# Optimization experiments

Hardware: AMD Instinct MI355X
Metric: run time of the kernel (lower is better)

## Reference

```python
import jax, jax.numpy as jnp
import numpy as np

EMB = 1024
HID = 4 * EMB
HEADS = 16
HEAD_DIM = EMB // HEADS


def gelu_tanh(x):
    c = jnp.sqrt(jnp.asarray(2.0 / jnp.pi, x.dtype))
    return 0.5 * x * (1.0 + jnp.tanh(c * (x + 0.044715 * x ** 3)))


def layernorm(x, scale, shift, eps=1e-5):
    mean = jnp.mean(x, axis=-1, keepdims=True)
    var = jnp.var(x, axis=-1, keepdims=True)
    return scale * (x - mean) / jnp.sqrt(var + eps) + shift


def setup_inputs() -> dict:
    key = jax.random.key(0)
    ks = jax.random.split(key, 12)
    s = 0.02
    return {
        "x": jax.random.normal(ks[0], (2, 2048, EMB), jnp.float32),
        "Wq": jax.random.normal(ks[1], (EMB, EMB), jnp.float32) * s,
        "Wk": jax.random.normal(ks[2], (EMB, EMB), jnp.float32) * s,
        "Wv": jax.random.normal(ks[3], (EMB, EMB), jnp.float32) * s,
        "Wo": jax.random.normal(ks[4], (EMB, EMB), jnp.float32) * s,
        "bo": jnp.zeros((EMB,), jnp.float32),
        "W1": jax.random.normal(ks[5], (EMB, HID), jnp.float32) * s,
        "b1": jnp.zeros((HID,), jnp.float32),
        "W2": jax.random.normal(ks[6], (HID, EMB), jnp.float32) * s,
        "b2": jnp.zeros((EMB,), jnp.float32),
        "ln1_scale": jnp.ones((EMB,), jnp.float32),
        "ln1_shift": jnp.zeros((EMB,), jnp.float32),
        "ln2_scale": jnp.ones((EMB,), jnp.float32),
        "ln2_shift": jnp.zeros((EMB,), jnp.float32),
    }


def reference(x, Wq, Wk, Wv, Wo, bo, W1, b1, W2, b2,
              ln1_scale, ln1_shift, ln2_scale, ln2_shift):
    B, S, D = x.shape

    # pre-norm attention + residual
    h = layernorm(x, ln1_scale, ln1_shift)
    q = (h @ Wq).reshape(B, S, HEADS, HEAD_DIM).transpose(0, 2, 1, 3)  # bhsd
    k = (h @ Wk).reshape(B, S, HEADS, HEAD_DIM).transpose(0, 2, 1, 3)
    v = (h @ Wv).reshape(B, S, HEADS, HEAD_DIM).transpose(0, 2, 1, 3)

    scores = jnp.einsum("bhqd,bhkd->bhqk", q, k)
    causal = jnp.tril(jnp.ones((S, S), bool))
    scores = jnp.where(causal, scores, -jnp.inf)
    attn = jax.nn.softmax(scores / jnp.sqrt(jnp.asarray(HEAD_DIM, x.dtype)), axis=-1)
    ctx = jnp.einsum("bhqk,bhkd->bhqd", attn, v)
    ctx = ctx.transpose(0, 2, 1, 3).reshape(B, S, D)
    x = x + (ctx @ Wo + bo)

    # pre-norm FFN + residual
    h = layernorm(x, ln2_scale, ln2_shift)
    h = gelu_tanh(h @ W1 + b1) @ W2 + b2
    return x + h
```

## Files before the change

kernel.cpp:

```cpp
#include <hip/hip_runtime.h>
#include <hip/hip_bf16.h>
#include <stdint.h>

#define B_   2
#define S_   2048
#define D_   1024
#define H_   16
#define DH_  64
#define HID_ 4096
#define M_   4096

typedef __bf16 bf16x8 __attribute__((ext_vector_type(8)));
typedef float  f32x4  __attribute__((ext_vector_type(4)));
typedef float  f32x16 __attribute__((ext_vector_type(16)));
typedef uint32_t u32x4v __attribute__((ext_vector_type(4)));

typedef const uint32_t __attribute__((address_space(1))) u32g;
typedef uint32_t       __attribute__((address_space(3))) u32l;

#define SCL2K_ 0.18033688011112042f

__device__ __forceinline__ uint16_t f2bf(float f) {
  uint32_t u = __builtin_bit_cast(uint32_t, f);
  u += 0x7FFFu + ((u >> 16) & 1u);
  return (uint16_t)(u >> 16);
}

__device__ __forceinline__ float bf2f(uint16_t u) {
  return __builtin_bit_cast(float, (uint32_t)u << 16);
}

__device__ __forceinline__ void gload_lds16(const void* g, void* l) {
  __builtin_amdgcn_global_load_lds((u32g*)g, (u32l*)l, 16, 0, 0);
}

__device__ __forceinline__ const bf16x8* lds8p(const uint16_t* base, int row,
                                               int cole) {
  int byt = (cole * 2) ^ ((row & 7) << 4);
  return reinterpret_cast<const bf16x8*>(base + row * 64 + (byt >> 1));
}

__device__ __forceinline__ const bf16x8* lds8p32(const uint16_t* base, int row,
                                                 int cole) {
  int byt = (cole * 2) ^ ((row & 7) << 4) ^ ((row & 8) << 2);
  return reinterpret_cast<const bf16x8*>(base + row * 64 + (byt >> 1));
}

__device__ __forceinline__ uint32_t cvtpk_bf16(float lo, float hi) {
  uint32_t d;
  asm("v_cvt_pk_bf16_f32 %0, %1, %2" : "=v"(d) : "v"(lo), "v"(hi));
  return d;
}
__device__ __forceinline__ void pl32swap(uint32_t& a, uint32_t& b) {
  asm volatile("v_permlane32_swap_b32 %0, %1" : "+v"(a), "+v"(b));
}

__global__ void wconv_t(const float* __restrict__ W, uint16_t* __restrict__ WT,
                        int K, int N) {
  __shared__ float tile[32][33];
  int n0 = blockIdx.x * 32, k0 = blockIdx.y * 32;
  int tx = threadIdx.x, ty = threadIdx.y;
#pragma unroll
  for (int i = 0; i < 4; ++i)
    tile[ty + i * 8][tx] = W[(size_t)(k0 + ty + i * 8) * N + n0 + tx];
  __syncthreads();
#pragma unroll
  for (int i = 0; i < 4; ++i)
    WT[(size_t)(n0 + ty + i * 8) * K + k0 + tx] = f2bf(tile[tx][ty + i * 8]);
}

__global__ __launch_bounds__(256) void ln_k(const float* __restrict__ x,
                                            const float* __restrict__ sc,
                                            const float* __restrict__ sh,
                                            uint16_t* __restrict__ out) {
  int row = blockIdx.x;
  int t = threadIdx.x;
  float4 v = reinterpret_cast<const float4*>(x + (size_t)row * D_)[t];
  float s = v.x + v.y + v.z + v.w;
  float ss = v.x * v.x + v.y * v.y + v.z * v.z + v.w * v.w;
#pragma unroll
  for (int off = 32; off >= 1; off >>= 1) {
    s += __shfl_xor(s, off);
    ss += __shfl_xor(ss, off);
  }
  __shared__ float red[8];
  int wid = t >> 6, lane = t & 63;
  if (lane == 0) { red[wid] = s; red[wid + 4] = ss; }
  __syncthreads();
  s = red[0] + red[1] + red[2] + red[3];
  ss = red[4] + red[5] + red[6] + red[7];
  float mean = s * (1.0f / D_);
  float var = ss * (1.0f / D_) - mean * mean;
  float rstd = rsqrtf(var + 1e-5f);
  float4 g = reinterpret_cast<const float4*>(sc)[t];
  float4 b = reinterpret_cast<const float4*>(sh)[t];
  ushort4 o;
  o.x = f2bf(g.x * (v.x - mean) * rstd + b.x);
  o.y = f2bf(g.y * (v.y - mean) * rstd + b.y);
  o.z = f2bf(g.z * (v.z - mean) * rstd + b.z);
  o.w = f2bf(g.w * (v.w - mean) * rstd + b.w);
  reinterpret_cast<ushort4*>(out + (size_t)row * D_)[t] = o;
}

__global__ __launch_bounds__(256) void reduce4_k(
    const uint16_t* __restrict__ P0, const uint16_t* __restrict__ P1,
    const uint16_t* __restrict__ P2, const uint16_t* __restrict__ P3,
    const float* __restrict__ resid, const float* __restrict__ bias,
    float* __restrict__ out) {
  int row = blockIdx.x, t = threadIdx.x;
  size_t base = (size_t)row * D_ + t * 4;
  float4 r = *reinterpret_cast<const float4*>(resid + base);
  float4 b = reinterpret_cast<const float4*>(bias)[t];
  ushort4 u0 = *reinterpret_cast<const ushort4*>(P0 + base);
  ushort4 u1 = *reinterpret_cast<const ushort4*>(P1 + base);
  ushort4 u2 = *reinterpret_cast<const ushort4*>(P2 + base);
  ushort4 u3 = *reinterpret_cast<const ushort4*>(P3 + base);
  float4 o;
  o.x = r.x + b.x + bf2f(u0.x) + bf2f(u1.x) + bf2f(u2.x) + bf2f(u3.x);
  o.y = r.y + b.y + bf2f(u0.y) + bf2f(u1.y) + bf2f(u2.y) + bf2f(u3.y);
  o.z = r.z + b.z + bf2f(u0.z) + bf2f(u1.z) + bf2f(u2.z) + bf2f(u3.z);
  o.w = r.w + b.w + bf2f(u0.w) + bf2f(u1.w) + bf2f(u2.w) + bf2f(u3.w);
  *reinterpret_cast<float4*>(out + base) = o;
}

__global__ void vtrans_k(const uint16_t* __restrict__ V, uint16_t* __restrict__ VT) {
  __shared__ uint16_t tile[32][33];
  int s0 = blockIdx.x * 32, d0 = blockIdx.y * 32, bh = blockIdx.z;
  int tx = threadIdx.x, ty = threadIdx.y;
  const uint16_t* vb = V + (size_t)bh * S_ * DH_;
  uint16_t* vtb = VT + (size_t)bh * DH_ * S_;
#pragma unroll
  for (int i = 0; i < 4; ++i)
    tile[ty + i * 8][tx] = vb[(size_t)(s0 + ty + i * 8) * DH_ + d0 + tx];
  __syncthreads();
#pragma unroll
  for (int i = 0; i < 4; ++i)
    vtb[(size_t)(d0 + ty + i * 8) * S_ + s0 + tx] = tile[tx][ty + i * 8];
}

template <int EPI>
__global__ __launch_bounds__(512, 2) void gemm8(
    const uint16_t* __restrict__ A, const uint16_t* __restrict__ BT,
    void* __restrict__ Cout, const float* __restrict__ bias,
    uint16_t* __restrict__ P0, uint16_t* __restrict__ P1,
    uint16_t* __restrict__ P2, uint16_t* __restrict__ P3,
    int M, int N, int K) {
  __shared__ uint16_t As[2][2][128 * 64];
  __shared__ uint16_t Bs[2][2][128 * 64];
  int t = threadIdx.x;
  int lane = t & 63, wid = t >> 6;
  int wm = wid >> 2, wn = wid & 3;
  int l15 = lane & 15, lk8 = (lane >> 4) * 8, lr4 = (lane >> 4) * 4;
  int gx = gridDim.x;
  int nwg = gx * gridDim.y;
  int bid = blockIdx.y * gx + blockIdx.x;
  int swz = (bid & 7) * (nwg >> 3) + (bid >> 3);
  int bx = swz % gx, by = swz / gx;
  int m0 = by * 256, n0 = bx * 256;
  int ksz = K / gridDim.z;
  int kbeg = blockIdx.z * ksz;
  int NT = ksz >> 6;

  int r0 = t >> 3, slot0 = t & 7;
  int scol = (slot0 ^ (r0 & 7)) * 8;

  auto STAGE_A = [&](int kt, int half, int buf) {
    const uint16_t* src =
        A + (size_t)(m0 + half * 128 + r0) * K + kbeg + kt * 64 + scol;
    uint16_t* dst = &As[buf][half][t * 8];
    gload_lds16(src, dst);
    gload_lds16(src + (size_t)64 * K, dst + 4096);
  };
  auto STAGE_B = [&](int kt, int half, int buf) {
    const uint16_t* src =
        BT + (size_t)(n0 + half * 128 + r0) * K + kbeg + kt * 64 + scol;
    uint16_t* dst = &Bs[buf][half][t * 8];
    gload_lds16(src, dst);
    gload_lds16(src + (size_t)64 * K, dst + 4096);
  };

  bf16x8 a[4][2], b[2][2];
  auto LDA = [&](int buf, int mh) {
#pragma unroll
    for (int j = 0; j < 4; ++j)
#pragma unroll
      for (int kk = 0; kk < 2; ++kk)
        a[j][kk] = *lds8p(As[buf][mh], wm * 64 + j * 16 + l15, kk * 32 + lk8);
  };
  auto LDB = [&](int buf, int nh) {
#pragma unroll
    for (int jj = 0; jj < 2; ++jj)
#pragma unroll
      for (int kk = 0; kk < 2; ++kk)
        b[jj][kk] = *lds8p(Bs[buf][nh], wn * 32 + jj * 16 + l15, kk * 32 + lk8);
  };

  f32x4 acc[8][4] = {};
  auto MM = [&](int mh, int nh) {
    __builtin_amdgcn_s_setprio(1);
#pragma unroll
    for (int kk = 0; kk < 2; ++kk)
#pragma unroll
      for (int j = 0; j < 4; ++j)
#pragma unroll
        for (int jj = 0; jj < 2; ++jj)
          acc[mh * 4 + j][nh * 2 + jj] = __builtin_amdgcn_mfma_f32_16x16x32_bf16(
              a[j][kk], b[jj][kk], acc[mh * 4 + j][nh * 2 + jj], 0, 0, 0);
    __builtin_amdgcn_s_setprio(0);
  };
  auto BAR = [&]() {
    __builtin_amdgcn_s_barrier();
    asm volatile("" ::: "memory");
  };
  auto LGKM0 = [&]() {
    asm volatile("s_waitcnt lgkmcnt(0)" ::: "memory");
    __builtin_amdgcn_sched_barrier(0);
  };

  STAGE_A(0, 0, 0);
  STAGE_B(0, 1, 0);
  STAGE_B(0, 0, 0);
  STAGE_A(0, 1, 0);
  STAGE_A(1, 0, 1);
  STAGE_B(1, 1, 1);
  asm volatile("s_waitcnt vmcnt(4)" ::: "memory");
  BAR();

  for (int T = 0; T < NT; ++T) {
    int cur = T & 1;
    LDA(cur, 0);
    LDB(cur, 0);
    if (T + 1 < NT) STAGE_B(T + 1, 0, cur ^ 1);
    BAR(); LGKM0();
    MM(0, 0);
    BAR();
    LDB(cur, 1);
    if (T + 1 < NT) STAGE_A(T + 1, 1, cur ^ 1);
    BAR(); LGKM0();
    MM(0, 1);
    BAR();
    LDA(cur, 1);
    if (T + 2 < NT) STAGE_A(T + 2, 0, cur);
    BAR(); LGKM0();
    MM(1, 1);
    BAR();
    LDB(cur, 0);
    if (T + 2 < NT) STAGE_B(T + 2, 1, cur);
    BAR(); LGKM0();
    MM(1, 0);
    if (T + 1 < NT) {
      if (T == NT - 2) {
        asm volatile("s_waitcnt vmcnt(0)" ::: "memory");
      } else {
        asm volatile("s_waitcnt vmcnt(4)" ::: "memory");
      }
    }
    BAR();
  }

  uint16_t* Pz = nullptr;
  if constexpr (EPI == 3) {
    int z = blockIdx.z;
    Pz = (z == 0) ? P0 : (z == 1) ? P1 : (z == 2) ? P2 : P3;
  }
#pragma unroll
  for (int mi = 0; mi < 8; ++mi) {
#pragma unroll
    for (int ni = 0; ni < 4; ++ni) {
#pragma unroll
      for (int rr = 0; rr < 4; ++rr) {
        int gm = m0 + (mi >> 2) * 128 + wm * 64 + (mi & 3) * 16 + lr4 + rr;
        int gn = n0 + (ni >> 1) * 128 + wn * 32 + (ni & 1) * 16 + l15;
        float v = acc[mi][ni][rr];
        if constexpr (EPI == 0) {
          int which = gn >> 10, nc = gn & 1023;
          int h = nc >> 6, dh = nc & 63;
          int bb = gm >> 11, s = gm & 2047;
          if (which == 1) v *= SCL2K_;
          ((uint16_t*)Cout)[((size_t)which * 32 + bb * 16 + h) * (S_ * 64) +
                            (size_t)s * 64 + dh] = f2bf(v);
        } else if constexpr (EPI == 2) {
          float u = v + bias[gn];
          float y = 0.7978845608028654f * (u + 0.044715f * u * u * u);
          float e = __expf(2.0f * y);
          float th = 1.0f - 2.0f / (e + 1.0f);
          ((uint16_t*)Cout)[(size_t)gm * N + gn] = f2bf(0.5f * u * (1.0f + th));
        } else {
          Pz[(size_t)gm * N + gn] = f2bf(v);
        }
      }
    }
  }
}

template <int EPI>
__global__ __launch_bounds__(256) void gemm_bt(
    const uint16_t* __restrict__ A, const uint16_t* __restrict__ BT,
    void* __restrict__ Cout, const float* __restrict__ bias,
    const float* __restrict__ resid, int M, int N, int K) {
  __shared__ uint16_t Asm_[128 * 64];
  __shared__ uint16_t Bsm_[128 * 64];
  int t = threadIdx.x;
  int lane = t & 63, wid = t >> 6;
  int wr = wid >> 1, wc = wid & 1;
  int nwg = gridDim.x * gridDim.y;
  int bid = blockIdx.y * gridDim.x + blockIdx.x;
  int swz = (bid & 7) * (nwg >> 3) + (bid >> 3);
  int bx = swz % gridDim.x, by = swz / gridDim.x;
  int m0 = by * 128, n0 = bx * 128;
  int l15 = lane & 15, lk8 = (lane >> 4) * 8;
  f32x4 acc[4][4] = {};

  auto STAGE = [&](int k0) {
#pragma unroll
    for (int it = 0; it < 4; ++it) {
      int idx = it * 256 + t;
      int r = idx >> 3, slot = idx & 7;
      int c = (slot ^ (r & 7)) * 8;
      gload_lds16(A + (size_t)(m0 + r) * K + k0 + c, &Asm_[idx * 8]);
      gload_lds16(BT + (size_t)(n0 + r) * K + k0 + c, &Bsm_[idx * 8]);
    }
  };

  int niter = K >> 6;
  for (int ki = 0; ki < niter; ++ki) {
    __syncthreads();
    STAGE(ki * 64);
    __syncthreads();
#pragma unroll
    for (int kk = 0; kk < 2; ++kk) {
      bf16x8 a[4], b[4];
#pragma unroll
      for (int mi = 0; mi < 4; ++mi)
        a[mi] = *lds8p(Asm_, wr * 64 + mi * 16 + l15, kk * 32 + lk8);
#pragma unroll
      for (int ni = 0; ni < 4; ++ni)
        b[ni] = *lds8p(Bsm_, wc * 64 + ni * 16 + l15, kk * 32 + lk8);
#pragma unroll
      for (int mi = 0; mi < 4; ++mi)
#pragma unroll
        for (int ni = 0; ni < 4; ++ni)
          acc[mi][ni] = __builtin_amdgcn_mfma_f32_16x16x32_bf16(
              a[mi], b[ni], acc[mi][ni], 0, 0, 0);
    }
  }
  int lr4 = (lane >> 4) * 4;
#pragma unroll
  for (int mi = 0; mi < 4; ++mi) {
#pragma unroll
    for (int ni = 0; ni < 4; ++ni) {
#pragma unroll
      for (int r = 0; r < 4; ++r) {
        int gm = m0 + wr * 64 + mi * 16 + lr4 + r;
        int gn = n0 + wc * 64 + ni * 16 + l15;
        float v = acc[mi][ni][r];
        if constexpr (EPI == 1) {
          ((float*)Cout)[(size_t)gm * N + gn] =
              resid[(size_t)gm * N + gn] + v + bias[gn];
        }
      }
    }
  }
}

__global__ __launch_bounds__(64) void attn32_k(const uint16_t* __restrict__ Q,
                                               const uint16_t* __restrict__ Kv,
                                               const uint16_t* __restrict__ VT,
                                               uint16_t* __restrict__ ctx) {
  __shared__ uint16_t Ksm[2][32 * 64];
  __shared__ uint16_t Vsm[2][32 * 64];
  __shared__ float invLDS[32];
  int bid = blockIdx.x;
  int qt = bid >> 5;
  int bh = bid & 31;
  int lane = threadIdx.x;
  int l31 = lane & 31, lh = lane >> 5;
  int b_ = bh >> 4, h_ = bh & 15;

  auto STAGE = [&](int k0, int bufi) {
#pragma unroll
    for (int c = 0; c < 4; ++c) {
      int idx = c * 64 + lane;
      int r = idx >> 3, sl = idx & 7;
      int slp = sl ^ (r & 7) ^ ((r & 8) >> 2);
      gload_lds16(Kv + ((size_t)bh * S_ + k0 + r) * 64 + slp * 8,
                  &Ksm[bufi][idx * 8]);
      int dh = 2 * r + (slp >> 2), ko = (slp & 3) * 8;
      gload_lds16(VT + ((size_t)bh * 64 + dh) * S_ + k0 + ko,
                  &Vsm[bufi][idx * 8]);
    }
  };

  int nkt = qt + 1;
  int qbase = qt * 32;
  bf16x8 qf[4];
#pragma unroll
  for (int dk = 0; dk < 4; ++dk)
    qf[dk] = *reinterpret_cast<const bf16x8*>(
        Q + ((size_t)bh * S_ + qbase + l31) * 64 + dk * 16 + lh * 8);
  f32x16 o0 = {}, o1 = {};
  float mrow = -3.0e38f, lsum = 0.0f;
  int buf = 0;
  STAGE(0, 0);

  for (int t = 0; t < nkt; ++t) {
    if (t + 1 < nkt) {
      STAGE((t + 1) * 32, buf ^ 1);
      asm volatile("s_waitcnt vmcnt(8)" ::: "memory");
    } else {
      asm volatile("s_waitcnt vmcnt(0)" ::: "memory");
    }
    __builtin_amdgcn_sched_barrier(0);
    f32x16 Sf = {};
#pragma unroll
    for (int dk = 0; dk < 4; ++dk) {
      bf16x8 kf = *lds8p32(Ksm[buf], l31, dk * 16 + lh * 8);
      Sf = __builtin_amdgcn_mfma_f32_32x32x16_bf16(kf, qf[dk], Sf, 0, 0, 0);
    }
    float sv[16];
    if (t == nkt - 1) {
#pragma unroll
      for (int rr = 0; rr < 16; ++rr) {
        int koff = (rr & 3) + 8 * (rr >> 2) + 4 * lh;
        sv[rr] = (koff <= l31) ? Sf[rr] : -3.0e38f;
      }
    } else {
#pragma unroll
      for (int rr = 0; rr < 16; ++rr) sv[rr] = Sf[rr];
    }
    float mt16 = sv[0];
#pragma unroll
    for (int rr = 1; rr < 16; ++rr) mt16 = fmaxf(mt16, sv[rr]);
    if (__any(mt16 > mrow + 8.0f)) {
      float mt = mt16;
#pragma unroll
      for (int off = 32; off >= 1; off >>= 1)
        mt = fmaxf(mt, __shfl_xor(mt, off));
      mt = fmaxf(mt, mrow);
      float fac = __builtin_amdgcn_exp2f(mrow - mt);
      mrow = mt;
      lsum *= fac;
#pragma unroll
      for (int rr = 0; rr < 16; ++rr) { o0[rr] *= fac; o1[rr] *= fac; }
    }
    float pv[16];
#pragma unroll
    for (int rr = 0; rr < 16; ++rr) {
      pv[rr] = __builtin_amdgcn_exp2f(sv[rr] - mrow);
      lsum += pv[rr];
    }
    uint32_t a0 = cvtpk_bf16(pv[0], pv[1]), b0 = cvtpk_bf16(pv[4], pv[5]);
    pl32swap(a0, b0);
    uint32_t a1 = cvtpk_bf16(pv[2], pv[3]), b1 = cvtpk_bf16(pv[6], pv[7]);
    pl32swap(a1, b1);
    u32x4v w0 = {a0, a1, b0, b1};
    bf16x8 pa0 = __builtin_bit_cast(bf16x8, w0);
    uint32_t a2 = cvtpk_bf16(pv[8], pv[9]), b2 = cvtpk_bf16(pv[12], pv[13]);
    pl32swap(a2, b2);
    uint32_t a3 = cvtpk_bf16(pv[10], pv[11]), b3 = cvtpk_bf16(pv[14], pv[15]);
    pl32swap(a3, b3);
    u32x4v w1 = {a2, a3, b2, b3};
    bf16x8 pa1 = __builtin_bit_cast(bf16x8, w1);
    int vrow = l31 >> 1, vcb = (l31 & 1) * 32 + lh * 8;
    bf16x8 v00 = *lds8p32(Vsm[buf], vrow, vcb);
    o0 = __builtin_amdgcn_mfma_f32_32x32x16_bf16(pa0, v00, o0, 0, 0, 0);
    bf16x8 v01 = *lds8p32(Vsm[buf], vrow, vcb + 16);
    o0 = __builtin_amdgcn_mfma_f32_32x32x16_bf16(pa1, v01, o0, 0, 0, 0);
    bf16x8 v10 = *lds8p32(Vsm[buf], 16 + vrow, vcb);
    o1 = __builtin_amdgcn_mfma_f32_32x32x16_bf16(pa0, v10, o1, 0, 0, 0);
    bf16x8 v11 = *lds8p32(Vsm[buf], 16 + vrow, vcb + 16);
    o1 = __builtin_amdgcn_mfma_f32_32x32x16_bf16(pa1, v11, o1, 0, 0, 0);
    buf ^= 1;
  }
  lsum += __shfl_xor(lsum, 32);
  if (lane < 32) invLDS[l31] = 1.0f / lsum;
  asm volatile("s_waitcnt lgkmcnt(0)" ::: "memory");
  __builtin_amdgcn_sched_barrier(0);
  float inv[16];
#pragma unroll
  for (int rr = 0; rr < 16; ++rr)
    inv[rr] = invLDS[(rr & 3) + 8 * (rr >> 2) + 4 * lh];
#pragma unroll
  for (int rr = 0; rr < 16; ++rr) {
    int s = qbase + (rr & 3) + 8 * (rr >> 2) + 4 * lh;
    size_t base = ((size_t)(b_ * S_ + s)) * D_ + h_ * 64;
    ctx[base + l31] = f2bf(o0[rr] * inv[rr]);
    ctx[base + 32 + l31] = f2bf(o1[rr] * inv[rr]);
  }
}

extern "C" void kernel_launch(void* const* d_in, const int* in_sizes, int n_in,
                              void* d_out, int out_size, void* d_ws, size_t ws_size,
                              hipStream_t stream) {
  const float* x    = (const float*)d_in[0];
  const float* Wq   = (const float*)d_in[1];
  const float* Wk   = (const float*)d_in[2];
  const float* Wv   = (const float*)d_in[3];
  const float* Wo   = (const float*)d_in[4];
  const float* bo   = (const float*)d_in[5];
  const float* W1   = (const float*)d_in[6];
  const float* b1   = (const float*)d_in[7];
  const float* W2   = (const float*)d_in[8];
  const float* b2   = (const float*)d_in[9];
  const float* ln1s = (const float*)d_in[10];
  const float* ln1b = (const float*)d_in[11];
  const float* ln2s = (const float*)d_in[12];
  const float* ln2b = (const float*)d_in[13];
  float* out = (float*)d_out;
  char* ws = (char*)d_ws;

  const size_t MB = 1024 * 1024;
  uint16_t* WQKVT = (uint16_t*)(ws + 0);
  uint16_t* WOT   = (uint16_t*)(ws + 6 * MB);
  uint16_t* W1T   = (uint16_t*)(ws + 8 * MB);
  uint16_t* W2T   = (uint16_t*)(ws + 16 * MB);
  uint16_t* H1    = (uint16_t*)(ws + 24 * MB);
  float*    X1    = (float*)(ws + 32 * MB);
  uint16_t* QKV   = (uint16_t*)(ws + 48 * MB);
  uint16_t* VTb   = (uint16_t*)(ws + 72 * MB);
  uint16_t* CTX   = (uint16_t*)(ws + 80 * MB);
  uint16_t* FFH   = (uint16_t*)(ws + 48 * MB);
  uint16_t* SP0   = (uint16_t*)(ws + 0);
  uint16_t* SP1   = (uint16_t*)(ws + 8 * MB);
  uint16_t* SP2   = (uint16_t*)(ws + 24 * MB);
  uint16_t* SP3   = (uint16_t*)(ws + 80 * MB);

  dim3 b32x8(32, 8);
  wconv_t<<<dim3(32, 32), b32x8, 0, stream>>>(Wq, WQKVT, 1024, 1024);
  wconv_t<<<dim3(32, 32), b32x8, 0, stream>>>(Wk, WQKVT + 1024 * 1024, 1024, 1024);
  wconv_t<<<dim3(32, 32), b32x8, 0, stream>>>(Wv, WQKVT + 2 * 1024 * 1024, 1024, 1024);
  wconv_t<<<dim3(32, 32), b32x8, 0, stream>>>(Wo, WOT, 1024, 1024);
  wconv_t<<<dim3(128, 32), b32x8, 0, stream>>>(W1, W1T, 1024, 4096);
  wconv_t<<<dim3(32, 128), b32x8, 0, stream>>>(W2, W2T, 4096, 1024);

  ln_k<<<M_, 256, 0, stream>>>(x, ln1s, ln1b, H1);
  gemm8<0><<<dim3(12, 16), 512, 0, stream>>>(H1, WQKVT, QKV, nullptr,
                                             nullptr, nullptr, nullptr, nullptr,
                                             M_, 3072, 1024);
  const uint16_t* Qp = QKV;
  const uint16_t* Kp = QKV + (size_t)32 * S_ * 64;
  const uint16_t* Vp = QKV + (size_t)64 * S_ * 64;
  vtrans_k<<<dim3(64, 2, 32), b32x8, 0, stream>>>(Vp, VTb);
  attn32_k<<<dim3(2048), 64, 0, stream>>>(Qp, Kp, VTb, CTX);
  gemm_bt<1><<<dim3(8, 32), 256, 0, stream>>>(CTX, WOT, X1, bo, x, M_, 1024, 1024);
  ln_k<<<M_, 256, 0, stream>>>(X1, ln2s, ln2b, H1);
  gemm8<2><<<dim3(16, 16), 512, 0, stream>>>(H1, W1T, FFH, b1,
                                             nullptr, nullptr, nullptr, nullptr,
                                             M_, 4096, 1024);
  gemm8<3><<<dim3(4, 16, 4), 512, 0, stream>>>(FFH, W2T, nullptr, nullptr,
                                               SP0, SP1, SP2, SP3,
                                               M_, 1024, 4096);
  reduce4_k<<<M_, 256, 0, stream>>>(SP0, SP1, SP2, SP3, X1, b2, out);
}
```

Baseline: 256.5 us.

## Split causal attention KV range across two blocks and merge partials; fuse weight conversions

Attention now splits each query tile's causal key range into two halves handled by separate blocks. Each block writes an unnormalized bf16 partial output plus its row max and sum, and a new combine kernel merges the pairs, which balances the triangular workload and doubles the block count. The attention loop also drops LDS staging in favour of direct register loads of K and V, double-buffered in registers. The six weight-transpose launches are merged into one kernel. The cost is an extra launch and round-trip of the partial outputs, plus rounding the unnormalized partials to bf16.

```diff
diff --git a/kernel.cpp b/kernel.cpp
--- a/kernel.cpp
+++ b/kernel.cpp
@@ -40,12 +40,6 @@
   return reinterpret_cast<const bf16x8*>(base + row * 64 + (byt >> 1));
 }
 
-__device__ __forceinline__ const bf16x8* lds8p32(const uint16_t* base, int row,
-                                                 int cole) {
-  int byt = (cole * 2) ^ ((row & 7) << 4) ^ ((row & 8) << 2);
-  return reinterpret_cast<const bf16x8*>(base + row * 64 + (byt >> 1));
-}
-
 __device__ __forceinline__ uint32_t cvtpk_bf16(float lo, float hi) {
   uint32_t d;
   asm("v_cvt_pk_bf16_f32 %0, %1, %2" : "=v"(d) : "v"(lo), "v"(hi));
@@ -55,10 +49,29 @@
   asm volatile("v_permlane32_swap_b32 %0, %1" : "+v"(a), "+v"(b));
 }
 
-__global__ void wconv_t(const float* __restrict__ W, uint16_t* __restrict__ WT,
-                        int K, int N) {
+__global__ void wconv_all(const float* __restrict__ Wq, const float* __restrict__ Wk,
+                          const float* __restrict__ Wv, const float* __restrict__ Wo,
+                          const float* __restrict__ W1, const float* __restrict__ W2,
+                          uint16_t* __restrict__ WQKVT, uint16_t* __restrict__ WOT,
+                          uint16_t* __restrict__ W1T, uint16_t* __restrict__ W2T) {
   __shared__ float tile[32][33];
-  int n0 = blockIdx.x * 32, k0 = blockIdx.y * 32;
+  int idx = blockIdx.x;
+  const float* W;
+  uint16_t* WT;
+  int K, N, within;
+  if (idx < 4096) {
+    int which = idx >> 10;
+    within = idx & 1023;
+    W = (which == 0) ? Wq : (which == 1) ? Wk : (which == 2) ? Wv : Wo;
+    WT = (which == 3) ? WOT : WQKVT + (size_t)which * 1024 * 1024;
+    K = 1024; N = 1024;
+  } else if (idx < 8192) {
+    within = idx - 4096; W = W1; WT = W1T; K = 1024; N = 4096;
+  } else {
+    within = idx - 8192; W = W2; WT = W2T; K = 4096; N = 1024;
+  }
+  int nb = N >> 5;
+  int n0 = (within % nb) * 32, k0 = (within / nb) * 32;
   int tx = threadIdx.x, ty = threadIdx.y;
 #pragma unroll
   for (int i = 0; i < 4; ++i)
@@ -363,129 +376,158 @@
   }
 }
 
-__global__ __launch_bounds__(64) void attn32_k(const uint16_t* __restrict__ Q,
-                                               const uint16_t* __restrict__ Kv,
-                                               const uint16_t* __restrict__ VT,
-                                               uint16_t* __restrict__ ctx) {
-  __shared__ uint16_t Ksm[2][32 * 64];
-  __shared__ uint16_t Vsm[2][32 * 64];
-  __shared__ float invLDS[32];
+__global__ __launch_bounds__(64) void attn32s_k(const uint16_t* __restrict__ Q,
+                                                const uint16_t* __restrict__ Kv,
+                                                const uint16_t* __restrict__ VT,
+                                                uint16_t* __restrict__ Obuf,
+                                                float* __restrict__ ML) {
   int bid = blockIdx.x;
-  int qt = bid >> 5;
   int bh = bid & 31;
+  int s = (bid >> 5) & 1;
+  int qt = bid >> 6;
   int lane = threadIdx.x;
   int l31 = lane & 31, lh = lane >> 5;
-  int b_ = bh >> 4, h_ = bh & 15;
-
-  auto STAGE = [&](int k0, int bufi) {
-#pragma unroll
-    for (int c = 0; c < 4; ++c) {
-      int idx = c * 64 + lane;
-      int r = idx >> 3, sl = idx & 7;
-      int slp = sl ^ (r & 7) ^ ((r & 8) >> 2);
-      gload_lds16(Kv + ((size_t)bh * S_ + k0 + r) * 64 + slp * 8,
-                  &Ksm[bufi][idx * 8]);
-      int dh = 2 * r + (slp >> 2), ko = (slp & 3) * 8;
-      gload_lds16(VT + ((size_t)bh * 64 + dh) * S_ + k0 + ko,
-                  &Vsm[bufi][idx * 8]);
-    }
-  };
-
   int nkt = qt + 1;
-  int qbase = qt * 32;
-  bf16x8 qf[4];
-#pragma unroll
-  for (int dk = 0; dk < 4; ++dk)
-    qf[dk] = *reinterpret_cast<const bf16x8*>(
-        Q + ((size_t)bh * S_ + qbase + l31) * 64 + dk * 16 + lh * 8);
+  int h = (nkt + 1) >> 1;
+  int t0 = s ? h : 0, t1 = s ? nkt : h;
+  int pb = ((qt * 32 + bh) << 1) + s;
+
   f32x16 o0 = {}, o1 = {};
   float mrow = -3.0e38f, lsum = 0.0f;
-  int buf = 0;
-  STAGE(0, 0);
-
-  for (int t = 0; t < nkt; ++t) {
-    if (t + 1 < nkt) {
-      STAGE((t + 1) * 32, buf ^ 1);
-      asm volatile("s_waitcnt vmcnt(8)" ::: "memory");
-    } else {
-      asm volatile("s_waitcnt vmcnt(0)" ::: "memory");
+
+  const uint16_t* Kb = Kv + (size_t)bh * S_ * 64;
+  const uint16_t* Vb = VT + (size_t)bh * 64 * S_;
+
+  auto LOADKV = [&](int t, bf16x8 (&kf)[4], bf16x8 (&vf)[4]) {
+    const uint16_t* kp = Kb + (size_t)(t * 32 + l31) * 64 + lh * 8;
+#pragma unroll
+    for (int dk = 0; dk < 4; ++dk)
+      kf[dk] = *reinterpret_cast<const bf16x8*>(kp + dk * 16);
+    const uint16_t* vp = Vb + (size_t)l31 * S_ + t * 32 + lh * 8;
+    vf[0] = *reinterpret_cast<const bf16x8*>(vp);
+    vf[1] = *reinterpret_cast<const bf16x8*>(vp + 16);
+    vf[2] = *reinterpret_cast<const bf16x8*>(vp + 32 * S_);
+    vf[3] = *reinterpret_cast<const bf16x8*>(vp + 32 * S_ + 16);
+  };
+
+  if (t0 < t1) {
+    int qbase = qt * 32;
+    bf16x8 qf[4];
+#pragma unroll
+    for (int dk = 0; dk < 4; ++dk)
+      qf[dk] = *reinterpret_cast<const bf16x8*>(
+          Q + ((size_t)bh * S_ + qbase + l31) * 64 + dk * 16 + lh * 8);
+
+    auto COMPUTE = [&](int t, bf16x8 (&kf)[4], bf16x8 (&vf)[4]) {
+      f32x16 Sf = {};
+#pragma unroll
+      for (int dk = 0; dk < 4; ++dk)
+        Sf = __builtin_amdgcn_mfma_f32_32x32x16_bf16(kf[dk], qf[dk], Sf, 0, 0, 0);
+      float sv[16];
+      if (t == qt) {
+#pragma unroll
+        for (int rr = 0; rr < 16; ++rr) {
+          int koff = (rr & 3) + 8 * (rr >> 2) + 4 * lh;
+          sv[rr] = (koff <= l31) ? Sf[rr] : -3.0e38f;
+        }
+      } else {
+#pragma unroll
+        for (int rr = 0; rr < 16; ++rr) sv[rr] = Sf[rr];
+      }
+      float mt16 = sv[0];
+#pragma unroll
+      for (int rr = 1; rr < 16; ++rr) mt16 = fmaxf(mt16, sv[rr]);
+      if (__any(mt16 > mrow + 8.0f)) {
+        float mt = mt16;
+#pragma unroll
+        for (int off = 32; off >= 1; off >>= 1)
+          mt = fmaxf(mt, __shfl_xor(mt, off));
+        mt = fmaxf(mt, mrow);
+        float fac = __builtin_amdgcn_exp2f(mrow - mt);
+        mrow = mt;
+        lsum *= fac;
+#pragma unroll
+        for (int rr = 0; rr < 16; ++rr) { o0[rr] *= fac; o1[rr] *= fac; }
+      }
+      float pv[16];
+#pragma unroll
+      for (int rr = 0; rr < 16; ++rr) {
+        pv[rr] = __builtin_amdgcn_exp2f(sv[rr] - mrow);
+        lsum += pv[rr];
+      }
+      uint32_t a0 = cvtpk_bf16(pv[0], pv[1]), b0 = cvtpk_bf16(pv[4], pv[5]);
+      pl32swap(a0, b0);
+      uint32_t a1 = cvtpk_bf16(pv[2], pv[3]), b1 = cvtpk_bf16(pv[6], pv[7]);
+      pl32swap(a1, b1);
+      u32x4v w0 = {a0, a1, b0, b1};
+      bf16x8 pa0 = __builtin_bit_cast(bf16x8, w0);
+      uint32_t a2 = cvtpk_bf16(pv[8], pv[9]), b2 = cvtpk_bf16(pv[12], pv[13]);
+      pl32swap(a2, b2);
+      uint32_t a3 = cvtpk_bf16(pv[10], pv[11]), b3 = cvtpk_bf16(pv[14], pv[15]);
+      pl32swap(a3, b3);
+      u32x4v w1 = {a2, a3, b2, b3};
+      bf16x8 pa1 = __builtin_bit_cast(bf16x8, w1);
+      o0 = __builtin_amdgcn_mfma_f32_32x32x16_bf16(pa0, vf[0], o0, 0, 0, 0);
+      o0 = __builtin_amdgcn_mfma_f32_32x32x16_bf16(pa1, vf[1], o0, 0, 0, 0);
+      o1 = __builtin_amdgcn_mfma_f32_32x32x16_bf16(pa0, vf[2], o1, 0, 0, 0);
+      o1 = __builtin_amdgcn_mfma_f32_32x32x16_bf16(pa1, vf[3], o1, 0, 0, 0);
+    };
+
+    bf16x8 kA[4], vA[4], kB[4], vB[4];
+    LOADKV(t0, kA, vA);
+    int t = t0;
+    while (t < t1) {
+      if (t + 1 < t1) LOADKV(t + 1, kB, vB);
+      COMPUTE(t, kA, vA);
+      ++t;
+      if (t >= t1) break;
+      if (t + 1 < t1) LOADKV(t + 1, kA, vA);
+      COMPUTE(t, kB, vB);
+      ++t;
     }
-    __builtin_amdgcn_sched_barrier(0);
-    f32x16 Sf = {};
-#pragma unroll
-    for (int dk = 0; dk < 4; ++dk) {
-      bf16x8 kf = *lds8p32(Ksm[buf], l31, dk * 16 + lh * 8);
-      Sf = __builtin_amdgcn_mfma_f32_32x32x16_bf16(kf, qf[dk], Sf, 0, 0, 0);
-    }
-    float sv[16];
-    if (t == nkt - 1) {
-#pragma unroll
-      for (int rr = 0; rr < 16; ++rr) {
-        int koff = (rr & 3) + 8 * (rr >> 2) + 4 * lh;
-        sv[rr] = (koff <= l31) ? Sf[rr] : -3.0e38f;
-      }
-    } else {
-#pragma unroll
-      for (int rr = 0; rr < 16; ++rr) sv[rr] = Sf[rr];
-    }
-    float mt16 = sv[0];
-#pragma unroll
-    for (int rr = 1; rr < 16; ++rr) mt16 = fmaxf(mt16, sv[rr]);
-    if (__any(mt16 > mrow + 8.0f)) {
-      float mt = mt16;
-#pragma unroll
-      for (int off = 32; off >= 1; off >>= 1)
-        mt = fmaxf(mt, __shfl_xor(mt, off));
-      mt = fmaxf(mt, mrow);
-      float fac = __builtin_amdgcn_exp2f(mrow - mt);
-      mrow = mt;
-      lsum *= fac;
-#pragma unroll
-      for (int rr = 0; rr < 16; ++rr) { o0[rr] *= fac; o1[rr] *= fac; }
-    }
-    float pv[16];
-#pragma unroll
-    for (int rr = 0; rr < 16; ++rr) {
-      pv[rr] = __builtin_amdgcn_exp2f(sv[rr] - mrow);
-      lsum += pv[rr];
-    }
-    uint32_t a0 = cvtpk_bf16(pv[0], pv[1]), b0 = cvtpk_bf16(pv[4], pv[5]);
-    pl32swap(a0, b0);
-    uint32_t a1 = cvtpk_bf16(pv[2], pv[3]), b1 = cvtpk_bf16(pv[6], pv[7]);
-    pl32swap(a1, b1);
-    u32x4v w0 = {a0, a1, b0, b1};
-    bf16x8 pa0 = __builtin_bit_cast(bf16x8, w0);
-    uint32_t a2 = cvtpk_bf16(pv[8], pv[9]), b2 = cvtpk_bf16(pv[12], pv[13]);
-    pl32swap(a2, b2);
-    uint32_t a3 = cvtpk_bf16(pv[10], pv[11]), b3 = cvtpk_bf16(pv[14], pv[15]);
-    pl32swap(a3, b3);
-    u32x4v w1 = {a2, a3, b2, b3};
-    bf16x8 pa1 = __builtin_bit_cast(bf16x8, w1);
-    int vrow = l31 >> 1, vcb = (l31 & 1) * 32 + lh * 8;
-    bf16x8 v00 = *lds8p32(Vsm[buf], vrow, vcb);
-    o0 = __builtin_amdgcn_mfma_f32_32x32x16_bf16(pa0, v00, o0, 0, 0, 0);
-    bf16x8 v01 = *lds8p32(Vsm[buf], vrow, vcb + 16);
-    o0 = __builtin_amdgcn_mfma_f32_32x32x16_bf16(pa1, v01, o0, 0, 0, 0);
-    bf16x8 v10 = *lds8p32(Vsm[buf], 16 + vrow, vcb);
-    o1 = __builtin_amdgcn_mfma_f32_32x32x16_bf16(pa0, v10, o1, 0, 0, 0);
-    bf16x8 v11 = *lds8p32(Vsm[buf], 16 + vrow, vcb + 16);
-    o1 = __builtin_amdgcn_mfma_f32_32x32x16_bf16(pa1, v11, o1, 0, 0, 0);
-    buf ^= 1;
-  }
-  lsum += __shfl_xor(lsum, 32);
-  if (lane < 32) invLDS[l31] = 1.0f / lsum;
-  asm volatile("s_waitcnt lgkmcnt(0)" ::: "memory");
-  __builtin_amdgcn_sched_barrier(0);
-  float inv[16];
-#pragma unroll
-  for (int rr = 0; rr < 16; ++rr)
-    inv[rr] = invLDS[(rr & 3) + 8 * (rr >> 2) + 4 * lh];
+    lsum += __shfl_xor(lsum, 32);
+  }
+
+  if (lane < 32) {
+    ML[(size_t)pb * 64 + l31 * 2] = mrow;
+    ML[(size_t)pb * 64 + l31 * 2 + 1] = lsum;
+  }
 #pragma unroll
   for (int rr = 0; rr < 16; ++rr) {
-    int s = qbase + (rr & 3) + 8 * (rr >> 2) + 4 * lh;
-    size_t base = ((size_t)(b_ * S_ + s)) * D_ + h_ * 64;
-    ctx[base + l31] = f2bf(o0[rr] * inv[rr]);
-    ctx[base + 32 + l31] = f2bf(o1[rr] * inv[rr]);
+    int srow = (rr & 3) + 8 * (rr >> 2) + 4 * lh;
+    size_t base = (size_t)pb * 2048 + srow * 64;
+    Obuf[base + l31] = f2bf(o0[rr]);
+    Obuf[base + 32 + l31] = f2bf(o1[rr]);
+  }
+}
+
+__global__ __launch_bounds__(64) void attncomb_k(const uint16_t* __restrict__ Obuf,
+                                                 const float* __restrict__ ML,
+                                                 uint16_t* __restrict__ ctx) {
+  int blk = blockIdx.x;
+  int qt = blk >> 5, bh = blk & 31;
+  int lane = threadIdx.x;
+  int q = lane >> 1, half = lane & 1;
+  size_t pb0 = (size_t)blk * 2, pb1 = pb0 + 1;
+  float m0 = ML[pb0 * 64 + q * 2], l0 = ML[pb0 * 64 + q * 2 + 1];
+  float m1 = ML[pb1 * 64 + q * 2], l1 = ML[pb1 * 64 + q * 2 + 1];
+  float m = fmaxf(m0, m1);
+  float w0 = __builtin_amdgcn_exp2f(m0 - m), w1 = __builtin_amdgcn_exp2f(m1 - m);
+  float invL = 1.0f / (l0 * w0 + l1 * w1);
+  int b_ = bh >> 4, h_ = bh & 15;
+  int srow = qt * 32 + q;
+  size_t ib = pb0 * 2048 + q * 64 + half * 32;
+  size_t ob = ((size_t)(b_ * S_ + srow)) * D_ + h_ * 64 + half * 32;
+#pragma unroll
+  for (int i = 0; i < 8; ++i) {
+    ushort4 u0 = *reinterpret_cast<const ushort4*>(Obuf + ib + i * 4);
+    ushort4 u1 = *reinterpret_cast<const ushort4*>(Obuf + 2048 + ib + i * 4);
+    ushort4 o;
+    o.x = f2bf((bf2f(u0.x) * w0 + bf2f(u1.x) * w1) * invL);
+    o.y = f2bf((bf2f(u0.y) * w0 + bf2f(u1.y) * w1) * invL);
+    o.z = f2bf((bf2f(u0.z) * w0 + bf2f(u1.z) * w1) * invL);
+    o.w = f2bf((bf2f(u0.w) * w0 + bf2f(u1.w) * w1) * invL);
+    *reinterpret_cast<ushort4*>(ctx + ob + i * 4) = o;
   }
 }
 
@@ -520,19 +562,16 @@
   uint16_t* VTb   = (uint16_t*)(ws + 72 * MB);
   uint16_t* CTX   = (uint16_t*)(ws + 80 * MB);
   uint16_t* FFH   = (uint16_t*)(ws + 48 * MB);
+  uint16_t* AOB   = (uint16_t*)(ws + 24 * MB);
+  float*    AML   = (float*)(ws + 40 * MB);
   uint16_t* SP0   = (uint16_t*)(ws + 0);
   uint16_t* SP1   = (uint16_t*)(ws + 8 * MB);
   uint16_t* SP2   = (uint16_t*)(ws + 24 * MB);
   uint16_t* SP3   = (uint16_t*)(ws + 80 * MB);
 
   dim3 b32x8(32, 8);
-  wconv_t<<<dim3(32, 32), b32x8, 0, stream>>>(Wq, WQKVT, 1024, 1024);
-  wconv_t<<<dim3(32, 32), b32x8, 0, stream>>>(Wk, WQKVT + 1024 * 1024, 1024, 1024);
-  wconv_t<<<dim3(32, 32), b32x8, 0, stream>>>(Wv, WQKVT + 2 * 1024 * 1024, 1024, 1024);
-  wconv_t<<<dim3(32, 32), b32x8, 0, stream>>>(Wo, WOT, 1024, 1024);
-  wconv_t<<<dim3(128, 32), b32x8, 0, stream>>>(W1, W1T, 1024, 4096);
-  wconv_t<<<dim3(32, 128), b32x8, 0, stream>>>(W2, W2T, 4096, 1024);
-
+  wconv_all<<<dim3(12288), b32x8, 0, stream>>>(Wq, Wk, Wv, Wo, W1, W2,
+                                               WQKVT, WOT, W1T, W2T);
   ln_k<<<M_, 256, 0, stream>>>(x, ln1s, ln1b, H1);
   gemm8<0><<<dim3(12, 16), 512, 0, stream>>>(H1, WQKVT, QKV, nullptr,
                                              nullptr, nullptr, nullptr, nullptr,
@@ -541,7 +580,8 @@
   const uint16_t* Kp = QKV + (size_t)32 * S_ * 64;
   const uint16_t* Vp = QKV + (size_t)64 * S_ * 64;
   vtrans_k<<<dim3(64, 2, 32), b32x8, 0, stream>>>(Vp, VTb);
-  attn32_k<<<dim3(2048), 64, 0, stream>>>(Qp, Kp, VTb, CTX);
+  attn32s_k<<<dim3(4096), 64, 0, stream>>>(Qp, Kp, VTb, AOB, AML);
+  attncomb_k<<<dim3(2048), 64, 0, stream>>>(AOB, AML, CTX);
   gemm_bt<1><<<dim3(8, 32), 256, 0, stream>>>(CTX, WOT, X1, bo, x, M_, 1024, 1024);
   ln_k<<<M_, 256, 0, stream>>>(X1, ln2s, ln2b, H1);
   gemm8<2><<<dim3(16, 16), 512, 0, stream>>>(H1, W1T, FFH, b1,
```

After: 260.7 us. No clear change (+1.6%).
